# Kernel optimization log

Measured on AMD Instinct MI355X. Metric: run time of the kernel, lower is better.

Reference implementation:

```python
import jax, jax.numpy as jnp
import numpy as np

MIN_PS = 4
MAX_PS = 16


def _enforce(mb):
    # mb: (L,) bool candidate boundaries (merge_signal < 0.7-quantile)
    # Faithful re-implementation of _enforce_patch_size_constraints:
    # walk boundaries left->right, skip segments < MIN_PS (start not advanced),
    # accept otherwise, and insert ceil(ps/MAX_PS)-1 evenly spaced splits for
    # oversized segments. seq_len-1 is always appended as a candidate.
    L = mb.shape[0]
    pos = jnp.arange(L, dtype=jnp.int32)
    cand = mb | (pos == L - 1)

    def fwd_step(start, inp):
        p, is_c = inp
        ps = p - start
        acc = is_c & (ps >= MIN_PS)
        k = jnp.where(acc, (ps + MAX_PS - 1) // MAX_PS, jnp.int32(1))
        sz = jnp.maximum(jnp.where(acc, ps // k, jnp.int32(1)), 1)
        new_start = jnp.where(acc, p, start)
        return new_start, (acc, start, sz, k)

    _, (acc, seg_start, sz, k) = jax.lax.scan(fwd_step, jnp.int32(0), (pos, cand))

    # Reverse scan: propagate each accepted boundary's (start, split_size, num_splits)
    # back to the interior positions of its segment so splits can be placed in parallel.
    def rev_step(carry, inp):
        a, s, z, kk = inp
        cs, cz, ck, cv = carry
        out = (cs, cz, ck, cv)
        ncarry = (jnp.where(a, s, cs), jnp.where(a, z, cz), jnp.where(a, kk, ck), cv | a)
        return ncarry, out

    init = (jnp.int32(0), jnp.int32(1), jnp.int32(1), jnp.bool_(False))
    _, (fs, fz, fk, fv) = jax.lax.scan(rev_step, init, (acc, seg_start, sz, k), reverse=True)
    r = pos - fs
    j = r // fz
    split = fv & (r > 0) & (r % fz == 0) & (j >= 1) & (j <= fk - 1)
    return acc | split


def reference(x, attention_mask, W1, b1, W2, b2, Wc, bc, Wb1, bb1, Wb2, bb2):
    B, L, D = x.shape
    # content scorer: Linear -> ReLU -> Linear -> Sigmoid
    content = jax.nn.sigmoid(jax.nn.relu(x @ W1 + b1) @ W2 + b2)[..., 0]  # (B, L)
    # grouped Conv1d(d, d//2, k=3, pad=1, groups=d//4)
    xc = jnp.transpose(x, (0, 2, 1))  # (B, D, L)
    pf = jax.lax.conv_general_dilated(xc, Wc, (1,), ((1, 1),),
                                      feature_group_count=D // 4,
                                      dimension_numbers=('NCH', 'OIH', 'NCH'))
    pf = jnp.transpose(pf + bc[None, :, None], (0, 2, 1))  # (B, L, D//2)
    comb = jnp.concatenate([x, pf], axis=-1)
    bscore = jax.nn.sigmoid(jax.nn.relu(comb @ Wb1 + bb1) @ Wb2 + bb2)[..., 0]  # (B, L)
    signal = content * (1.0 - bscore) * attention_mask
    thr = jnp.quantile(signal, 0.7, axis=1, keepdims=True)
    mb = signal < thr
    new_b = jax.vmap(_enforce)(mb)  # (B, L) bool, new_b[:,0] is always False

    # segment id per token = inclusive cumsum of boundaries
    seg = jnp.cumsum(new_b.astype(jnp.int32), axis=1)
    seg_flat = (seg + jnp.arange(B, dtype=jnp.int32)[:, None] * L).reshape(-1)
    NS = B * L
    xm = x * attention_mask[..., None]
    e = jnp.sum(xm * xm, axis=-1).reshape(-1)  # softmax logits = ||token||^2
    m = jax.ops.segment_max(e, seg_flat, num_segments=NS)
    w = jnp.exp(e - m[seg_flat])
    denom = jax.ops.segment_sum(w, seg_flat, num_segments=NS)
    wn = w / denom[seg_flat]
    merged = jax.ops.segment_sum(xm.reshape(-1, D) * wn[:, None], seg_flat,
                                 num_segments=NS).reshape(B, L, D)
    # segment_boundaries: 1 for every segment except the first, zero padding
    n_last = seg[:, -1]
    p = jnp.arange(L)
    seg_bounds = ((p[None, :] >= 1) & (p[None, :] <= n_last[:, None])).astype(jnp.float32)
    return merged, seg_bounds


def setup_inputs() -> dict:
    key = jax.random.key(0)
    B, L, D = 4, 8192, 512
    ks = jax.random.split(key, 8)
    s = 0.02
    return {
        'x': jax.random.normal(ks[0], (B, L, D), jnp.float32),
        'attention_mask': jnp.ones((B, L), jnp.float32),
        'W1': jax.random.normal(ks[1], (D, D // 4), jnp.float32) * s,
        'b1': jnp.zeros((D // 4,), jnp.float32),
        'W2': jax.random.normal(ks[2], (D // 4, 1), jnp.float32) * s,
        'b2': jnp.zeros((1,), jnp.float32),
        'Wc': jax.random.normal(ks[3], (D // 2, 4, 3), jnp.float32) * s,
        'bc': jnp.zeros((D // 2,), jnp.float32),
        'Wb1': jax.random.normal(ks[4], (D + D // 2, D // 4), jnp.float32) * s,
        'bb1': jnp.zeros((D // 4,), jnp.float32),
        'Wb2': jax.random.normal(ks[5], (D // 4, 1), jnp.float32) * s,
        'bb2': jnp.zeros((1,), jnp.float32),
    }
```

## Files before the change

kernel.cpp:

```cpp
#include <hip/hip_runtime.h>
#include <math.h>

#define B_  4
#define L_  8192
#define D_  512
#define BL_ (B_*L_)
#define TOK 64
#define XS  68
#define KC  16
#define NCH (D_/KC)

__global__ __launch_bounds__(256, 2) void k_signal(
    const float* __restrict__ x, const float* __restrict__ mask,
    const float* __restrict__ W1, const float* __restrict__ b1,
    const float* __restrict__ W2, const float* __restrict__ b2,
    const float* __restrict__ Wc, const float* __restrict__ bc,
    const float* __restrict__ Wb1, const float* __restrict__ bb1,
    const float* __restrict__ Wb2, const float* __restrict__ bb2,
    float* __restrict__ signal, float* __restrict__ e)
{
  __shared__ float ws1[KC][128];
  __shared__ float wsb[KC][128];
  __shared__ float wsp[8][128];
  __shared__ float xt[KC][XS];
  __shared__ float pf[8][XS];

  const int t   = threadIdx.x;
  const int blk = blockIdx.x;
  const int b   = blk >> 7;
  const int l0  = (blk & 127) << 6;
  const float* xb = x + (size_t)b * L_ * D_;

  const int jq = t & 31, tw = t >> 5;
  const int j0 = jq << 2, tok0 = tw << 3;

  const int stok = t >> 2, skk = t & 3;
  const int oo_c = t >> 5;
  const int m2   = (t & 31) << 1;
  const int cb_c = (oo_c >> 1) << 2;

  const int srow = t >> 5, sc4 = (t & 31) << 2;

  float a1[8][4], a2[8][4];
#pragma unroll
  for (int i = 0; i < 8; ++i)
#pragma unroll
    for (int j = 0; j < 4; ++j) { a1[i][j] = 0.f; a2[i][j] = 0.f; }
  float esacc = 0.f;

  float4 r_w1a, r_w1b, r_wba, r_wbb, r_wp, r_xv, r_hv;
  float4 r_wc0, r_wc1, r_wc2;
  float  r_bc;

  auto LOAD = [&](int c) {
    const int kc = c << 4;
    r_w1a = *reinterpret_cast<const float4*>(W1  + (size_t)(kc + srow) * 128 + sc4);
    r_w1b = *reinterpret_cast<const float4*>(W1  + (size_t)(kc + 8 + srow) * 128 + sc4);
    r_wba = *reinterpret_cast<const float4*>(Wb1 + (size_t)(kc + srow) * 128 + sc4);
    r_wbb = *reinterpret_cast<const float4*>(Wb1 + (size_t)(kc + 8 + srow) * 128 + sc4);
    r_wp  = *reinterpret_cast<const float4*>(Wb1 + (size_t)(512 + (c << 3) + srow) * 128 + sc4);
    r_xv  = *reinterpret_cast<const float4*>(xb + (size_t)(l0 + stok) * D_ + kc + (skk << 2));
    if (t < 8) {
      const int hh = t >> 2, kk = t & 3;
      const int l = hh ? (l0 + TOK) : (l0 - 1);
      r_hv = make_float4(0.f, 0.f, 0.f, 0.f);
      if (l >= 0 && l < L_)
        r_hv = *reinterpret_cast<const float4*>(xb + (size_t)l * D_ + kc + (kk << 2));
    }
    const int o = (c << 3) + oo_c;
    const float* wcp = Wc + o * 12;
    r_wc0 = *reinterpret_cast<const float4*>(wcp);
    r_wc1 = *reinterpret_cast<const float4*>(wcp + 4);
    r_wc2 = *reinterpret_cast<const float4*>(wcp + 8);
    r_bc  = bc[o];
  };

  LOAD(0);

  for (int c = 0; c < NCH; ++c) {
    __syncthreads();

    *reinterpret_cast<float4*>(&ws1[srow][sc4])     = r_w1a;
    *reinterpret_cast<float4*>(&ws1[8 + srow][sc4]) = r_w1b;
    *reinterpret_cast<float4*>(&wsb[srow][sc4])     = r_wba;
    *reinterpret_cast<float4*>(&wsb[8 + srow][sc4]) = r_wbb;
    *reinterpret_cast<float4*>(&wsp[srow][sc4])     = r_wp;
    {
      const float4 v = r_xv;
      esacc = fmaf(v.x, v.x, esacc); esacc = fmaf(v.y, v.y, esacc);
      esacc = fmaf(v.z, v.z, esacc); esacc = fmaf(v.w, v.w, esacc);
      const int r = skk << 2;
      xt[r + 0][stok] = v.x; xt[r + 1][stok] = v.y;
      xt[r + 2][stok] = v.z; xt[r + 3][stok] = v.w;
    }
    if (t < 8) {
      const int hh = t >> 2, kk = t & 3;
      const int col = TOK + hh, r = kk << 2;
      xt[r + 0][col] = r_hv.x; xt[r + 1][col] = r_hv.y;
      xt[r + 2][col] = r_hv.z; xt[r + 3][col] = r_hv.w;
    }
    __syncthreads();

    float wcl[12];
    wcl[0] = r_wc0.x; wcl[1]  = r_wc0.y; wcl[2]  = r_wc0.z; wcl[3]  = r_wc0.w;
    wcl[4] = r_wc1.x; wcl[5]  = r_wc1.y; wcl[6]  = r_wc1.z; wcl[7]  = r_wc1.w;
    wcl[8] = r_wc2.x; wcl[9]  = r_wc2.y; wcl[10] = r_wc2.z; wcl[11] = r_wc2.w;
    const float bcv = r_bc;

    if (c + 1 < NCH) LOAD(c + 1);

    {
      float pa = bcv, pb = bcv;
      const int tm1 = (m2 == 0) ? TOK : m2 - 1;
      const int tp2 = (m2 + 2 == TOK) ? TOK + 1 : m2 + 2;
#pragma unroll
      for (int i = 0; i < 4; ++i) {
        const float* row = &xt[cb_c + i][0];
        const float  xm1 = row[tm1];
        const float2 x01 = *reinterpret_cast<const float2*>(&row[m2]);
        const float  xp2 = row[tp2];
        pa = fmaf(xm1,   wcl[i * 3 + 0], pa);
        pa = fmaf(x01.x, wcl[i * 3 + 1], pa);
        pa = fmaf(x01.y, wcl[i * 3 + 2], pa);
        pb = fmaf(x01.x, wcl[i * 3 + 0], pb);
        pb = fmaf(x01.y, wcl[i * 3 + 1], pb);
        pb = fmaf(xp2,   wcl[i * 3 + 2], pb);
      }
      *reinterpret_cast<float2*>(&pf[oo_c][m2]) = make_float2(pa, pb);
    }

#pragma unroll 4
    for (int k = 0; k < KC; ++k) {
      const float4 w1 = *reinterpret_cast<const float4*>(&ws1[k][j0]);
      const float4 wb = *reinterpret_cast<const float4*>(&wsb[k][j0]);
      const float4 xa = *reinterpret_cast<const float4*>(&xt[k][tok0]);
      const float4 xc = *reinterpret_cast<const float4*>(&xt[k][tok0 + 4]);
      const float xs8[8] = {xa.x, xa.y, xa.z, xa.w, xc.x, xc.y, xc.z, xc.w};
#pragma unroll
      for (int i = 0; i < 8; ++i) {
        a1[i][0] = fmaf(xs8[i], w1.x, a1[i][0]);
        a1[i][1] = fmaf(xs8[i], w1.y, a1[i][1]);
        a1[i][2] = fmaf(xs8[i], w1.z, a1[i][2]);
        a1[i][3] = fmaf(xs8[i], w1.w, a1[i][3]);
        a2[i][0] = fmaf(xs8[i], wb.x, a2[i][0]);
        a2[i][1] = fmaf(xs8[i], wb.y, a2[i][1]);
        a2[i][2] = fmaf(xs8[i], wb.z, a2[i][2]);
        a2[i][3] = fmaf(xs8[i], wb.w, a2[i][3]);
      }
    }
    __syncthreads();

#pragma unroll 2
    for (int oo = 0; oo < 8; ++oo) {
      const float4 wp = *reinterpret_cast<const float4*>(&wsp[oo][j0]);
      const float4 pa4 = *reinterpret_cast<const float4*>(&pf[oo][tok0]);
      const float4 pb4 = *reinterpret_cast<const float4*>(&pf[oo][tok0 + 4]);
      const float ps8[8] = {pa4.x, pa4.y, pa4.z, pa4.w, pb4.x, pb4.y, pb4.z, pb4.w};
#pragma unroll
      for (int i = 0; i < 8; ++i) {
        a2[i][0] = fmaf(ps8[i], wp.x, a2[i][0]);
        a2[i][1] = fmaf(ps8[i], wp.y, a2[i][1]);
        a2[i][2] = fmaf(ps8[i], wp.z, a2[i][2]);
        a2[i][3] = fmaf(ps8[i], wp.w, a2[i][3]);
      }
    }
  }

  {
    float b1v[4], w2v[4], bbv[4], wv2[4];
#pragma unroll
    for (int jj = 0; jj < 4; ++jj) {
      b1v[jj] = b1[j0 + jj];  w2v[jj] = W2[j0 + jj];
      bbv[jj] = bb1[j0 + jj]; wv2[jj] = Wb2[j0 + jj];
    }
    const float bias2 = b2[0], biasb2 = bb2[0];
#pragma unroll
    for (int i = 0; i < 8; ++i) {
      float p1 = 0.f, p2 = 0.f;
#pragma unroll
      for (int jj = 0; jj < 4; ++jj) {
        const float h1 = a1[i][jj] + b1v[jj];
        if (h1 > 0.f) p1 = fmaf(h1, w2v[jj], p1);
        const float h2 = a2[i][jj] + bbv[jj];
        if (h2 > 0.f) p2 = fmaf(h2, wv2[jj], p2);
      }
#pragma unroll
      for (int off = 1; off < 32; off <<= 1) {
        p1 += __shfl_xor(p1, off, 64);
        p2 += __shfl_xor(p2, off, 64);
      }
      if (jq == 0) {
        const int gi = b * L_ + l0 + tok0 + i;
        const float content = 1.f / (1.f + expf(-(p1 + bias2)));
        const float bscore  = 1.f / (1.f + expf(-(p2 + biasb2)));
        signal[gi] = content * (1.f - bscore) * mask[gi];
      }
    }
  }

  {
    float es = esacc;
    es += __shfl_xor(es, 1, 64);
    es += __shfl_xor(es, 2, 64);
    if (skk == 0) {
      const int gi = b * L_ + l0 + stok;
      const float m = mask[gi];
      e[gi] = m * m * es;
    }
  }
}

__device__ __forceinline__ int chain_sim(unsigned long long w, int from) {
  int last = -1;
  while (from < 64) {
    const unsigned long long m = w & (~0ull << from);
    if (m == 0ull) break;
    const int p = __ffsll(m) - 1;
    last = p;
    from = p + 4;
  }
  return last;
}

__global__ __launch_bounds__(1024) void k_select(
    const float* __restrict__ signal,
    int* __restrict__ starts, int* __restrict__ nlast, float* __restrict__ bounds)
{
  __shared__ unsigned int bins[4][256];
  __shared__ unsigned int sel_prefix;
  __shared__ int sel_rank;
  __shared__ float sh_thr;
  __shared__ unsigned int wmin[16];
  __shared__ int wcnt[16];
  __shared__ unsigned long long cw[128];
  __shared__ unsigned char nb[L_];
  __shared__ signed char tbl[128][4];
  __shared__ int st_in[128];
  __shared__ int tsum[256];
  __shared__ int offs[257];

  const int b = blockIdx.x, t = threadIdx.x;
  const int wv = t >> 6, lane = t & 63;
  const float* s = signal + b * L_;

  float val[8];
  unsigned int key[8];
#pragma unroll
  for (int i = 0; i < 8; ++i) {
    val[i] = s[(i << 10) + t];
    const unsigned int u = __float_as_uint(val[i]);
    key[i] = (u & 0x80000000u) ? ~u : (u | 0x80000000u);
  }

  if (t == 0) { sel_prefix = 0u; sel_rank = 5733; }
  __syncthreads();
  for (int round = 0; round < 4; ++round) {
    reinterpret_cast<unsigned int*>(bins)[t] = 0u;
    __syncthreads();
    const unsigned int pre = sel_prefix;
    const int shift = 24 - 8 * round;
#pragma unroll
    for (int i = 0; i < 8; ++i) {
      if (round == 0 || (key[i] >> (shift + 8)) == pre)
        atomicAdd(&bins[t >> 8][(key[i] >> shift) & 255u], 1u);
    }
    __syncthreads();
    if (t < 256)
      bins[0][t] = bins[0][t] + bins[1][t] + bins[2][t] + bins[3][t];
    __syncthreads();
    if (t < 64) {
      const unsigned int c0 = bins[0][(t << 2) + 0], c1 = bins[0][(t << 2) + 1];
      const unsigned int c2 = bins[0][(t << 2) + 2], c3 = bins[0][(t << 2) + 3];
      const unsigned int lsum = c0 + c1 + c2 + c3;
      unsigned int run = lsum;
#pragma unroll
      for (int off = 1; off < 64; off <<= 1) {
        const unsigned int v = __shfl_up(run, off, 64);
        if (t >= off) run += v;
      }
      const int r = sel_rank;
      if (r >= (int)(run - lsum) && r < (int)run) {
        int rr = r - (int)(run - lsum);
        unsigned int cbin;
        if (rr < (int)c0) { cbin = 0; }
        else if (rr < (int)(c0 + c1)) { cbin = 1; rr -= (int)c0; }
        else if (rr < (int)(c0 + c1 + c2)) { cbin = 2; rr -= (int)(c0 + c1); }
        else { cbin = 3; rr -= (int)(c0 + c1 + c2); }
        sel_rank = rr;
        sel_prefix = (pre << 8) | ((unsigned int)(t << 2) | cbin);
      }
    }
    __syncthreads();
  }
  const unsigned int k0 = sel_prefix;

  {
    int cle = 0;
    unsigned int mgt = 0xFFFFFFFFu;
#pragma unroll
    for (int i = 0; i < 8; ++i) {
      if (key[i] <= k0) ++cle;
      else mgt = min(mgt, key[i]);
    }
#pragma unroll
    for (int off = 1; off < 64; off <<= 1) {
      cle += __shfl_xor(cle, off, 64);
      mgt = min(mgt, (unsigned int)__shfl_xor((int)mgt, off, 64));
    }
    if (lane == 0) { wcnt[wv] = cle; wmin[wv] = mgt; }
    __syncthreads();
    if (t == 0) {
      int C = 0; unsigned int M = 0xFFFFFFFFu;
      for (int g = 0; g < 16; ++g) { C += wcnt[g]; M = min(M, wmin[g]); }
      const unsigned int k1 = (C >= 5735) ? k0 : M;
      const unsigned int u0 = (k0 & 0x80000000u) ? (k0 & 0x7fffffffu) : ~k0;
      const unsigned int u1 = (k1 & 0x80000000u) ? (k1 & 0x7fffffffu) : ~k1;
      const float v0 = __uint_as_float(u0);
      const float v1 = __uint_as_float(u1);
      const float g = 0.7f * 8191.0f - 5733.0f;
      sh_thr = v0 + g * (v1 - v0);
    }
    __syncthreads();
  }
  const float thr = sh_thr;

#pragma unroll
  for (int i = 0; i < 8; ++i) {
    const unsigned long long m = __ballot(val[i] < thr);
    if (lane == 0) cw[(i << 4) + wv] = m;
  }
  {
    const int base = t << 3;
#pragma unroll
    for (int i = 0; i < 8; ++i) nb[base + i] = 0;
  }
  __syncthreads();
  if (t == 0) cw[127] |= (1ull << 63);
  __syncthreads();

  if (t < 512) {
    const int blk = t >> 2, cls = t & 3;
    tbl[blk][cls] = (signed char)chain_sim(cw[blk], cls);
  }
  __syncthreads();

  if (t == 0) {
    int st = 0;
    for (int blk = 0; blk < 128; ++blk) {
      const int bs = blk << 6;
      st_in[blk] = st;
      int pl;
      if (blk == 0) {
        pl = chain_sim(cw[0], 4);
      } else {
        int off = st + 4 - bs;
        if (off < 0) off = 0;
        pl = tbl[blk][off];
      }
      if (pl >= 0) st = bs + pl;
    }
  }
  __syncthreads();

  if (t < 128) {
    const int bs = t << 6;
    const unsigned long long w = cw[t];
    int st = st_in[t];
    int from = st + 4 - bs;
    if (from < 0) from = 0;
    while (from < 64) {
      const unsigned long long m = w & (~0ull << from);
      if (m == 0ull) break;
      const int p_rel = __ffsll(m) - 1;
      const int p = bs + p_rel;
      nb[p] = 1;
      const int ps = p - st;
      const int k = (ps + 15) >> 4;
      if (k > 1) {
        int sz = ps / k; if (sz < 1) sz = 1;
        for (int j = 1; j < k; ++j) nb[st + j * sz] = 1;
      }
      st = p;
      from = p_rel + 4;
    }
  }
  __syncthreads();

  if (t < 256) {
    const int base = t << 5;
    int ls = 0;
    for (int i = 0; i < 32; ++i) ls += nb[base + i];
    tsum[t] = ls;
  }
  __syncthreads();
  if (t == 0) {
    int r = 0;
    for (int i = 0; i < 256; ++i) { offs[i] = r; r += tsum[i]; }
    offs[256] = r;
  }
  __syncthreads();
  if (t < 256) {
    const int base = t << 5;
    int run = offs[t];
    for (int i = 0; i < 32; ++i) {
      run += nb[base + i];
      if (nb[base + i]) starts[b * L_ + run] = base + i;
    }
  }
  if (t == 0) { starts[b * L_ + 0] = 0; nlast[b] = offs[256]; }
  __syncthreads();
  const int total = offs[256];
  for (int i = t; i < L_; i += 1024)
    bounds[b * L_ + i] = (i >= 1 && i <= total) ? 1.0f : 0.0f;
}

__global__ __launch_bounds__(64) void k_merge(const float* __restrict__ x,
    const float* __restrict__ mask, const float* __restrict__ e,
    const int* __restrict__ starts, const int* __restrict__ nlast,
    float* __restrict__ merged)
{
  const int idx = blockIdx.x;
  const int b   = idx >> 13;
  const int sid = idx & (L_ - 1);
  const int n = nlast[b];
  const int lane = threadIdx.x;
  const int c0 = lane << 3;
  float* o = merged + (size_t)(b * L_ + sid) * D_ + c0;
  if (sid > n) {
    const float4 z = make_float4(0.f, 0.f, 0.f, 0.f);
    reinterpret_cast<float4*>(o)[0] = z;
    reinterpret_cast<float4*>(o)[1] = z;
    return;
  }
  const int t0 = starts[b * L_ + sid];
  const int t1 = (sid < n) ? starts[b * L_ + sid + 1] : L_;
  const float* eb = e + b * L_;

  float mx = -INFINITY;
  for (int p = t0; p < t1; ++p) mx = fmaxf(mx, eb[p]);
  float den = 0.f;
  for (int p = t0; p < t1; ++p) den += expf(eb[p] - mx);

  float acc[8] = {0,0,0,0,0,0,0,0};
  for (int p = t0; p < t1; ++p) {
    const float wn = expf(eb[p] - mx) / den;
    const float sc = wn * mask[b * L_ + p];
    const float* xr = x + ((size_t)(b * L_ + p)) * D_ + c0;
    const float4 u0 = reinterpret_cast<const float4*>(xr)[0];
    const float4 u1 = reinterpret_cast<const float4*>(xr)[1];
    acc[0] = fmaf(sc, u0.x, acc[0]); acc[1] = fmaf(sc, u0.y, acc[1]);
    acc[2] = fmaf(sc, u0.z, acc[2]); acc[3] = fmaf(sc, u0.w, acc[3]);
    acc[4] = fmaf(sc, u1.x, acc[4]); acc[5] = fmaf(sc, u1.y, acc[5]);
    acc[6] = fmaf(sc, u1.z, acc[6]); acc[7] = fmaf(sc, u1.w, acc[7]);
  }
  reinterpret_cast<float4*>(o)[0] = make_float4(acc[0], acc[1], acc[2], acc[3]);
  reinterpret_cast<float4*>(o)[1] = make_float4(acc[4], acc[5], acc[6], acc[7]);
}

extern "C" void kernel_launch(void* const* d_in, const int* in_sizes, int n_in,
                              void* d_out, int out_size, void* d_ws, size_t ws_size,
                              hipStream_t stream) {
  (void)in_sizes; (void)n_in; (void)out_size; (void)ws_size;
  const float* x    = (const float*)d_in[0];
  const float* mask = (const float*)d_in[1];
  const float* W1   = (const float*)d_in[2];
  const float* b1   = (const float*)d_in[3];
  const float* W2   = (const float*)d_in[4];
  const float* b2   = (const float*)d_in[5];
  const float* Wc   = (const float*)d_in[6];
  const float* bc   = (const float*)d_in[7];
  const float* Wb1  = (const float*)d_in[8];
  const float* bb1  = (const float*)d_in[9];
  const float* Wb2  = (const float*)d_in[10];
  const float* bb2  = (const float*)d_in[11];

  float* merged = (float*)d_out;
  float* bounds = (float*)d_out + (size_t)BL_ * D_;

  char* ws = (char*)d_ws;
  float* signal = (float*)(ws);
  float* e      = (float*)(ws + (size_t)BL_ * 4);
  int*   starts = (int*)  (ws + (size_t)BL_ * 8);
  int*   nlast  = (int*)  (ws + (size_t)BL_ * 12);

  k_signal<<<BL_ / TOK, 256, 0, stream>>>(x, mask, W1, b1, W2, b2, Wc, bc,
                                          Wb1, bb1, Wb2, bb2, signal, e);
  k_select<<<B_, 1024, 0, stream>>>(signal, starts, nlast, bounds);
  k_merge<<<BL_, 64, 0, stream>>>(x, mask, e, starts, nlast, merged);
}
```

Before: 304.6 us.

## Read MLP weights as wave-uniform scalar loads and pack four merge segments per block

The k_signal GEMM no longer stages W1/Wb1 tiles in shared memory. Each lane now owns one token, and each wave owns 32 hidden columns chosen by a readfirstlane-uniform offset, so weight reads can become scalar (SMEM) loads broadcast across the wave. The cross-wave output reduction moves to a small LDS buffer. This removes LDS weight traffic and a register-staged prefetch, but the scalar weight loads are no longer software-pipelined and may stall. Separately, k_merge packs four 64-thread segments into one 256-thread block to cut block launch overhead.

Result: slower. 499.6 us (+64.0%).

```diff
diff --git a/kernel.cpp b/kernel.cpp
--- a/kernel.cpp
+++ b/kernel.cpp
@@ -19,11 +19,10 @@
     const float* __restrict__ Wb2, const float* __restrict__ bb2,
     float* __restrict__ signal, float* __restrict__ e)
 {
-  __shared__ float ws1[KC][128];
-  __shared__ float wsb[KC][128];
-  __shared__ float wsp[8][128];
   __shared__ float xt[KC][XS];
   __shared__ float pf[8][XS];
+  __shared__ float red1[4][TOK];
+  __shared__ float red2[4][TOK];
 
   const int t   = threadIdx.x;
   const int blk = blockIdx.x;
@@ -31,35 +30,27 @@
   const int l0  = (blk & 127) << 6;
   const float* xb = x + (size_t)b * L_ * D_;
 
-  const int jq = t & 31, tw = t >> 5;
-  const int j0 = jq << 2, tok0 = tw << 3;
+  const int lane = t & 63;
+  const int wv   = t >> 6;
+  const int wj   = __builtin_amdgcn_readfirstlane(wv << 5);
 
   const int stok = t >> 2, skk = t & 3;
   const int oo_c = t >> 5;
   const int m2   = (t & 31) << 1;
   const int cb_c = (oo_c >> 1) << 2;
 
-  const int srow = t >> 5, sc4 = (t & 31) << 2;
-
-  float a1[8][4], a2[8][4];
-#pragma unroll
-  for (int i = 0; i < 8; ++i)
-#pragma unroll
-    for (int j = 0; j < 4; ++j) { a1[i][j] = 0.f; a2[i][j] = 0.f; }
+  float a1[32], a2[32];
+#pragma unroll
+  for (int j = 0; j < 32; ++j) { a1[j] = 0.f; a2[j] = 0.f; }
   float esacc = 0.f;
 
-  float4 r_w1a, r_w1b, r_wba, r_wbb, r_wp, r_xv, r_hv;
+  float4 r_xv, r_hv;
   float4 r_wc0, r_wc1, r_wc2;
   float  r_bc;
 
   auto LOAD = [&](int c) {
     const int kc = c << 4;
-    r_w1a = *reinterpret_cast<const float4*>(W1  + (size_t)(kc + srow) * 128 + sc4);
-    r_w1b = *reinterpret_cast<const float4*>(W1  + (size_t)(kc + 8 + srow) * 128 + sc4);
-    r_wba = *reinterpret_cast<const float4*>(Wb1 + (size_t)(kc + srow) * 128 + sc4);
-    r_wbb = *reinterpret_cast<const float4*>(Wb1 + (size_t)(kc + 8 + srow) * 128 + sc4);
-    r_wp  = *reinterpret_cast<const float4*>(Wb1 + (size_t)(512 + (c << 3) + srow) * 128 + sc4);
-    r_xv  = *reinterpret_cast<const float4*>(xb + (size_t)(l0 + stok) * D_ + kc + (skk << 2));
+    r_xv = *reinterpret_cast<const float4*>(xb + (size_t)(l0 + stok) * D_ + kc + (skk << 2));
     if (t < 8) {
       const int hh = t >> 2, kk = t & 3;
       const int l = hh ? (l0 + TOK) : (l0 - 1);
@@ -78,13 +69,9 @@
   LOAD(0);
 
   for (int c = 0; c < NCH; ++c) {
-    __syncthreads();
-
-    *reinterpret_cast<float4*>(&ws1[srow][sc4])     = r_w1a;
-    *reinterpret_cast<float4*>(&ws1[8 + srow][sc4]) = r_w1b;
-    *reinterpret_cast<float4*>(&wsb[srow][sc4])     = r_wba;
-    *reinterpret_cast<float4*>(&wsb[8 + srow][sc4]) = r_wbb;
-    *reinterpret_cast<float4*>(&wsp[srow][sc4])     = r_wp;
+    const int kc = c << 4;
+    __syncthreads();
+
     {
       const float4 v = r_xv;
       esacc = fmaf(v.x, v.x, esacc); esacc = fmaf(v.y, v.y, esacc);
@@ -129,72 +116,60 @@
       *reinterpret_cast<float2*>(&pf[oo_c][m2]) = make_float2(pa, pb);
     }
 
-#pragma unroll 4
-    for (int k = 0; k < KC; ++k) {
-      const float4 w1 = *reinterpret_cast<const float4*>(&ws1[k][j0]);
-      const float4 wb = *reinterpret_cast<const float4*>(&wsb[k][j0]);
-      const float4 xa = *reinterpret_cast<const float4*>(&xt[k][tok0]);
-      const float4 xc = *reinterpret_cast<const float4*>(&xt[k][tok0 + 4]);
-      const float xs8[8] = {xa.x, xa.y, xa.z, xa.w, xc.x, xc.y, xc.z, xc.w};
-#pragma unroll
-      for (int i = 0; i < 8; ++i) {
-        a1[i][0] = fmaf(xs8[i], w1.x, a1[i][0]);
-        a1[i][1] = fmaf(xs8[i], w1.y, a1[i][1]);
-        a1[i][2] = fmaf(xs8[i], w1.z, a1[i][2]);
-        a1[i][3] = fmaf(xs8[i], w1.w, a1[i][3]);
-        a2[i][0] = fmaf(xs8[i], wb.x, a2[i][0]);
-        a2[i][1] = fmaf(xs8[i], wb.y, a2[i][1]);
-        a2[i][2] = fmaf(xs8[i], wb.z, a2[i][2]);
-        a2[i][3] = fmaf(xs8[i], wb.w, a2[i][3]);
-      }
-    }
-    __syncthreads();
-
-#pragma unroll 2
-    for (int oo = 0; oo < 8; ++oo) {
-      const float4 wp = *reinterpret_cast<const float4*>(&wsp[oo][j0]);
-      const float4 pa4 = *reinterpret_cast<const float4*>(&pf[oo][tok0]);
-      const float4 pb4 = *reinterpret_cast<const float4*>(&pf[oo][tok0 + 4]);
-      const float ps8[8] = {pa4.x, pa4.y, pa4.z, pa4.w, pb4.x, pb4.y, pb4.z, pb4.w};
-#pragma unroll
-      for (int i = 0; i < 8; ++i) {
-        a2[i][0] = fmaf(ps8[i], wp.x, a2[i][0]);
-        a2[i][1] = fmaf(ps8[i], wp.y, a2[i][1]);
-        a2[i][2] = fmaf(ps8[i], wp.z, a2[i][2]);
-        a2[i][3] = fmaf(ps8[i], wp.w, a2[i][3]);
+    {
+      const float* w1c = W1  + (size_t)kc * 128 + wj;
+      const float* wbc = Wb1 + (size_t)kc * 128 + wj;
+#pragma unroll
+      for (int k = 0; k < KC; ++k) {
+        const float xv = xt[k][lane];
+        const float* w1r = w1c + (k << 7);
+        const float* wbr = wbc + (k << 7);
+#pragma unroll
+        for (int j = 0; j < 32; ++j) {
+          a1[j] = fmaf(xv, w1r[j], a1[j]);
+          a2[j] = fmaf(xv, wbr[j], a2[j]);
+        }
+      }
+    }
+    __syncthreads();
+
+    {
+      const float* wpc = Wb1 + (size_t)(512 + (c << 3)) * 128 + wj;
+#pragma unroll
+      for (int oo = 0; oo < 8; ++oo) {
+        const float pv = pf[oo][lane];
+        const float* wpr = wpc + (oo << 7);
+#pragma unroll
+        for (int j = 0; j < 32; ++j)
+          a2[j] = fmaf(pv, wpr[j], a2[j]);
       }
     }
   }
 
   {
-    float b1v[4], w2v[4], bbv[4], wv2[4];
-#pragma unroll
-    for (int jj = 0; jj < 4; ++jj) {
-      b1v[jj] = b1[j0 + jj];  w2v[jj] = W2[j0 + jj];
-      bbv[jj] = bb1[j0 + jj]; wv2[jj] = Wb2[j0 + jj];
-    }
-    const float bias2 = b2[0], biasb2 = bb2[0];
-#pragma unroll
-    for (int i = 0; i < 8; ++i) {
-      float p1 = 0.f, p2 = 0.f;
-#pragma unroll
-      for (int jj = 0; jj < 4; ++jj) {
-        const float h1 = a1[i][jj] + b1v[jj];
-        if (h1 > 0.f) p1 = fmaf(h1, w2v[jj], p1);
-        const float h2 = a2[i][jj] + bbv[jj];
-        if (h2 > 0.f) p2 = fmaf(h2, wv2[jj], p2);
-      }
-#pragma unroll
-      for (int off = 1; off < 32; off <<= 1) {
-        p1 += __shfl_xor(p1, off, 64);
-        p2 += __shfl_xor(p2, off, 64);
-      }
-      if (jq == 0) {
-        const int gi = b * L_ + l0 + tok0 + i;
-        const float content = 1.f / (1.f + expf(-(p1 + bias2)));
-        const float bscore  = 1.f / (1.f + expf(-(p2 + biasb2)));
-        signal[gi] = content * (1.f - bscore) * mask[gi];
-      }
+    float p1 = 0.f, p2 = 0.f;
+    const float* b1p  = b1  + wj;
+    const float* w2p  = W2  + wj;
+    const float* bbp  = bb1 + wj;
+    const float* wv2p = Wb2 + wj;
+#pragma unroll
+    for (int j = 0; j < 32; ++j) {
+      const float h1 = a1[j] + b1p[j];
+      if (h1 > 0.f) p1 = fmaf(h1, w2p[j], p1);
+      const float h2 = a2[j] + bbp[j];
+      if (h2 > 0.f) p2 = fmaf(h2, wv2p[j], p2);
+    }
+    __syncthreads();
+    red1[wv][lane] = p1;
+    red2[wv][lane] = p2;
+    __syncthreads();
+    if (wv == 0) {
+      const float q1 = ((red1[0][lane] + red1[1][lane]) + red1[2][lane]) + red1[3][lane];
+      const float q2 = ((red2[0][lane] + red2[1][lane]) + red2[2][lane]) + red2[3][lane];
+      const int gi = b * L_ + l0 + lane;
+      const float content = 1.f / (1.f + expf(-(q1 + b2[0])));
+      const float bscore  = 1.f / (1.f + expf(-(q2 + bb2[0])));
+      signal[gi] = content * (1.f - bscore) * mask[gi];
     }
   }
 
@@ -414,16 +389,16 @@
     bounds[b * L_ + i] = (i >= 1 && i <= total) ? 1.0f : 0.0f;
 }
 
-__global__ __launch_bounds__(64) void k_merge(const float* __restrict__ x,
+__global__ __launch_bounds__(256) void k_merge(const float* __restrict__ x,
     const float* __restrict__ mask, const float* __restrict__ e,
     const int* __restrict__ starts, const int* __restrict__ nlast,
     float* __restrict__ merged)
 {
-  const int idx = blockIdx.x;
+  const int idx = (blockIdx.x << 2) + (threadIdx.x >> 6);
   const int b   = idx >> 13;
   const int sid = idx & (L_ - 1);
   const int n = nlast[b];
-  const int lane = threadIdx.x;
+  const int lane = threadIdx.x & 63;
   const int c0 = lane << 3;
   float* o = merged + (size_t)(b * L_ + sid) * D_ + c0;
   if (sid > n) {
@@ -486,5 +461,5 @@
   k_signal<<<BL_ / TOK, 256, 0, stream>>>(x, mask, W1, b1, W2, b2, Wc, bc,
                                           Wb1, bb1, Wb2, bb2, signal, e);
   k_select<<<B_, 1024, 0, stream>>>(signal, starts, nlast, bounds);
-  k_merge<<<BL_, 64, 0, stream>>>(x, mask, e, starts, nlast, merged);
+  k_merge<<<BL_ / 4, 256, 0, stream>>>(x, mask, e, starts, nlast, merged);
 }
```
